# Kernel optimization log

Measured on AMD Instinct MI355X. Metric: run time of the kernel, lower is better.

The kernel has to match this reference:

```python
import jax, jax.numpy as jnp
import numpy as np
from jax import lax

D_MODEL, D_STATE, DT_RANK, D_INNER, K = 96, 16, 6, 192, 4


def cross_scan(x):
    # x: (B, C, H, W) -> (B, 4, C, L)
    B, C, H, W = x.shape
    x0 = x.reshape(B, C, H * W)                         # row-major scan
    x1 = jnp.transpose(x, (0, 1, 3, 2)).reshape(B, C, H * W)  # column-major scan
    return jnp.stack([x0, x1, x0[..., ::-1], x1[..., ::-1]], axis=1)


def cross_merge(ys, H, W):
    # ys: (B, 4, D, L) -> (B, D, L)
    B, Kd, D, L = ys.shape
    ys = ys[:, 0:2] + ys[:, 2:4, :, ::-1]
    y1 = jnp.transpose(ys[:, 1].reshape(B, D, W, H), (0, 1, 3, 2)).reshape(B, D, L)
    return ys[:, 0] + y1


def selective_scan(u, delta, A, Bs, Cs, Ds, delta_bias):
    # u, delta: (B, K, D, L); A: (K, D, N); Bs, Cs: (B, K, N, L); Ds, delta_bias: (K, D)
    Bsz, Kd, Dm, L = u.shape
    N = A.shape[-1]
    delta = jax.nn.softplus(delta + delta_bias[None, :, :, None])
    du = delta * u
    d_l = jnp.moveaxis(delta, -1, 0)   # (L, B, K, D)
    du_l = jnp.moveaxis(du, -1, 0)
    b_l = jnp.moveaxis(Bs, -1, 0)      # (L, B, K, N)
    c_l = jnpp = jnp.moveaxis(Cs, -1, 0)

    def step(h, inp):
        d_t, du_t, b_t, c_t = inp
        h = jnp.exp(d_t[..., None] * A) * h + du_t[..., None] * b_t[:, :, None, :]
        y = jnp.einsum('bkdn,bkn->bkd', h, c_t)
        return h, y

    h0 = jnp.zeros((Bsz, Kd, Dm, N), u.dtype)
    _, ys = lax.scan(step, h0, (d_l, du_l, b_l, c_l))
    ys = jnp.moveaxis(ys, 0, -1)  # (B, K, D, L)
    return ys + Ds[None, :, :, None] * u


def _forward(x, in_proj_w, conv_w, conv_b, x_proj_w, dt_projs_w, dt_projs_b,
             A_logs, Ds, out_norm_w, out_norm_b, out_proj_w):
    Bsz, H, W, dm = x.shape
    d_in = conv_w.shape[0]
    R, N = dt_projs_w.shape[2], A_logs.shape[-1]
    L = H * W
    # in_proj (no bias), split into x and gate z
    xz = jnp.einsum('bhwc,oc->bhwo', x, in_proj_w)
    xpart, z = jnp.split(xz, 2, axis=-1)
    z = jax.nn.silu(z)
    # depthwise 3x3 conv (NCHW) + SiLU
    xc = jnp.transpose(xpart, (0, 3, 1, 2))
    xc = lax.conv_general_dilated(xc, conv_w, (1, 1), 'SAME',
                                  feature_group_count=d_in,
                                  dimension_numbers=('NCHW', 'OIHW', 'NCHW'))
    xc = jax.nn.silu(xc + conv_b[None, :, None, None])
    # 4-directional cross scan
    xs = cross_scan(xc)                                   # (B, 4, d_in, L)
    x_dbl = jnp.einsum('bkdl,kcd->bkcl', xs, x_proj_w)    # (B, 4, R+2N, L)
    dts = jnp.einsum('bkrl,kdr->bkdl', x_dbl[:, :, :R], dt_projs_w)
    Bs = x_dbl[:, :, R:R + N]
    Cs = x_dbl[:, :, R + N:]
    A = -jnp.exp(A_logs)                                  # (4, d_in, N)
    ys = selective_scan(xs, dts, A, Bs, Cs, Ds, dt_projs_b)
    y = cross_merge(ys, H, W)                             # (B, d_in, L)
    y = jnp.transpose(y.reshape(Bsz, d_in, H, W), (0, 2, 3, 1))
    # out_norm = LayerNorm(d_inner), eps=1e-5
    mu = y.mean(-1, keepdims=True)
    var = ((y - mu) ** 2).mean(-1, keepdims=True)
    y = (y - mu) / jnp.sqrt(var + 1e-5) * out_norm_w + out_norm_b
    y = y * z
    return jnp.einsum('bhwd,od->bhwo', y, out_proj_w)


def setup_inputs() -> dict:
    key = jax.random.key(0)
    ks = jax.random.split(key, 8)
    dm, d_in, N, R = D_MODEL, D_INNER, D_STATE, DT_RANK
    x = jax.random.normal(ks[0], (8, 64, 64, dm), jnp.float32)
    in_proj_w = jax.random.normal(ks[1], (2 * d_in, dm), jnp.float32) * 0.02
    conv_w = jax.random.normal(ks[2], (d_in, 1, 3, 3), jnp.float32) * 0.1
    conv_b = jnp.zeros((d_in,), jnp.float32)
    x_proj_w = jax.random.normal(ks[3], (K, R + 2 * N, d_in), jnp.float32) * 0.02
    dt_projs_w = jax.random.normal(ks[4], (K, d_in, R), jnp.float32) * 0.1
    dt_projs_b = jax.random.uniform(ks[5], (K, d_in), jnp.float32, minval=-4.0, maxval=-2.0)
    A_logs = jnp.log(jnp.tile(jnp.arange(1, N + 1, dtype=jnp.float32)[None, None, :], (K, d_in, 1)))
    Ds = jnp.ones((K, d_in), jnp.float32)
    out_norm_w = jnp.ones((d_in,), jnp.float32)
    out_norm_b = jnp.zeros((d_in,), jnp.float32)
    out_proj_w = jax.random.normal(ks[6], (dm, d_in), jnp.float32) * 0.02
    return dict(x=x, in_proj_w=in_proj_w, conv_w=conv_w, conv_b=conv_b,
                x_proj_w=x_proj_w, dt_projs_w=dt_projs_w, dt_projs_b=dt_projs_b,
                A_logs=A_logs, Ds=Ds, out_norm_w=out_norm_w, out_norm_b=out_norm_b,
                out_proj_w=out_proj_w)


def reference(x, in_proj_w, conv_w, conv_b, x_proj_w, dt_projs_w, dt_projs_b,
              A_logs, Ds, out_norm_w, out_norm_b, out_proj_w):
    return _forward(x, in_proj_w, conv_w, conv_b, x_proj_w, dt_projs_w, dt_projs_b,
                    A_logs, Ds, out_norm_w, out_norm_b, out_proj_w)
```

## Files before the change

### kernel.cpp

```cpp
#include <hip/hip_runtime.h>
#include <math.h>

#define B_SZ 8
#define Hh 64
#define Ww 64
#define L 4096
#define Dm 96
#define Din 192
#define Kd 4
#define Ns 16
#define CPROJ 38
#define ROWW 40
#define NCHUNK 128
#define CHUNK 32

__device__ __forceinline__ float siluf_(float x){ return x / (1.f + __expf(-x)); }

__global__ void prep_kernel(const float* __restrict__ inw,
                            const float* __restrict__ xpw,
                            const float* __restrict__ outw,
                            float* __restrict__ wt_in,
                            float* __restrict__ wt_x,
                            float* __restrict__ wt_out){
  int i = blockIdx.x * blockDim.x + threadIdx.x;
  if (i < Dm*2*Din){ int k = i/(2*Din); int o = i%(2*Din); wt_in[i] = inw[o*Dm + k]; }
  int j = i - Dm*2*Din;
  if (j >= 0 && j < Din*Kd*CPROJ){ int k = j/(Kd*CPROJ); int c = j%(Kd*CPROJ); wt_x[j] = xpw[c*Din + k]; }
  int l = j - Din*Kd*CPROJ;
  if (l >= 0 && l < Din*Dm){ int dd = l/Dm; int o = l%Dm; wt_out[l] = outw[o*Din + dd]; }
}

__global__ __launch_bounds__(256) void zero_kernel(float4* __restrict__ p, int n4){
  int i = blockIdx.x * 256 + threadIdx.x;
  if (i < n4) p[i] = make_float4(0.f,0.f,0.f,0.f);
}

template<int KDIM, int OREAL, int EPI>
__global__ __launch_bounds__(256) void gemm_kernel(const float* __restrict__ X,
    const float* __restrict__ W, float* __restrict__ out0, float* __restrict__ out1){
  __shared__ float4 xt[128*24];
  const int tid = threadIdx.x;
  const int pg = tid & 15, og = tid >> 4;
  const int pblk = blockIdx.x & 255;
  const int oblk = blockIdx.x >> 8;
  const int p0 = pblk * 128;
  const bool act = (oblk*128 + og*8) < OREAL;
  int oc = oblk*128 + og*8;
  if (oc > OREAL-8) oc = OREAL-8;
  const int sw = pg & 7;

  float acc[8][8];
  #pragma unroll
  for (int i=0;i<8;i++){
    #pragma unroll
    for (int j2=0;j2<8;j2++) acc[i][j2] = 0.f;
  }

  for (int kp = 0; kp < KDIM/96; ++kp){
    __syncthreads();
    for (int idx = tid; idx < 128*24; idx += 256){
      int pp = idx/24, k4 = idx%24;
      size_t prow;
      if (EPI == 1){
        int b = pblk >> 5, tau = pblk & 31;
        int h = ((tau>>2)<<3) + (pp>>4);
        int w = ((tau&3)<<4) + (pp&15);
        prow = (size_t)b*L + h*64 + w;
      } else prow = (size_t)p0 + pp;
      float4 v = *(const float4*)&X[prow*KDIM + (size_t)kp*96 + k4*4];
      xt[pp*24 + (k4 ^ (pp&7))] = v;
    }
    __syncthreads();

    if (act){
      for (int k4 = 0; k4 < 24; ++k4){
        float4 wv[8];
        #pragma unroll
        for (int kk=0;kk<4;kk++){
          const float* wr = &W[(size_t)(kp*96 + k4*4 + kk)*OREAL + oc];
          wv[kk*2]   = *(const float4*)wr;
          wv[kk*2+1] = *(const float4*)(wr+4);
        }
        float4 xv[8];
        #pragma unroll
        for (int i=0;i<8;i++) xv[i] = xt[(pg+16*i)*24 + (k4 ^ sw)];
        #pragma unroll
        for (int kk=0;kk<4;kk++){
          const float4 wa = wv[kk*2], wb = wv[kk*2+1];
          #pragma unroll
          for (int i=0;i<8;i++){
            const float xk = ((const float*)&xv[i])[kk];
            acc[i][0] += xk*wa.x; acc[i][1] += xk*wa.y; acc[i][2] += xk*wa.z; acc[i][3] += xk*wa.w;
            acc[i][4] += xk*wb.x; acc[i][5] += xk*wb.y; acc[i][6] += xk*wb.z; acc[i][7] += xk*wb.w;
          }
        }
      }
    }
  }

  if (!act) return;
  if (EPI == 0){
    #pragma unroll
    for (int i=0;i<8;i++){
      size_t p = (size_t)p0 + pg + 16*i;
      if (oc < Din){
        *(float4*)&out0[p*Din + oc]     = make_float4(acc[i][0],acc[i][1],acc[i][2],acc[i][3]);
        *(float4*)&out0[p*Din + oc + 4] = make_float4(acc[i][4],acc[i][5],acc[i][6],acc[i][7]);
      } else {
        int zo = oc - Din;
        *(float4*)&out1[p*Din + zo]     = make_float4(siluf_(acc[i][0]),siluf_(acc[i][1]),siluf_(acc[i][2]),siluf_(acc[i][3]));
        *(float4*)&out1[p*Din + zo + 4] = make_float4(siluf_(acc[i][4]),siluf_(acc[i][5]),siluf_(acc[i][6]),siluf_(acc[i][7]));
      }
    }
  } else {
    const int b = pblk >> 5, tau = pblk & 31;
    #pragma unroll
    for (int i=0;i<8;i++){
      int q = pg + 16*i;
      int h = ((tau>>2)<<3) + (q>>4);
      int w = ((tau&3)<<4) + (q&15);
      int hw = h*64 + w;
      int t1 = ((hw&63)<<6) | (hw>>6);
      #pragma unroll
      for (int j2=0;j2<8;j2++){
        int c = oc + j2;
        int kd = c / CPROJ; int cc = c - kd*CPROJ;
        int t = (kd==0)? hw : (kd==1)? t1 : (kd==2)? (L-1-hw) : (L-1-t1);
        int dcol = (cc < 6) ? (32+cc) : (cc-6);
        out0[((size_t)(b*Kd+kd)*L + t)*ROWW + dcol] = acc[i][j2];
      }
    }
  }
}

__global__ __launch_bounds__(256) void conv_kernel(const float* __restrict__ xp,
    const float* __restrict__ cw, const float* __restrict__ cb, float* __restrict__ u){
  const int gid = blockIdx.x * 256 + threadIdx.x;
  const int d = gid % Din; const int p = gid / Din;
  const int b = p / L; const int hw = p % L; const int h = hw >> 6; const int w = hw & 63;
  float acc = cb[d];
  #pragma unroll
  for (int i=-1;i<=1;i++){
    const int hh = h + i; if (hh < 0 || hh >= Hh) continue;
    #pragma unroll
    for (int j=-1;j<=1;j++){
      const int ww = w + j; if (ww < 0 || ww >= Ww) continue;
      acc += xp[((size_t)(b*L + hh*Ww + ww))*Din + d] * cw[d*9 + (i+1)*3 + (j+1)];
    }
  }
  u[(size_t)p*Din + d] = siluf_(acc);
}

__device__ __forceinline__ void affine_pos(int k, int t0, int& gp0, int& gstr){
  if (k == 0){ gp0 = t0; gstr = 1; }
  else if (k == 1){ gp0 = ((t0 & 63) << 6) | (t0 >> 6); gstr = 64; }
  else if (k == 2){ gp0 = L-1-t0; gstr = -1; }
  else { const int T0 = L-1-t0; gp0 = ((T0 & 63) << 6) | (T0 >> 6); gstr = -64; }
}

__device__ __forceinline__ void ladder_(float e1, float* e){
  e[0]=e1;
  #pragma unroll
  for (int n=1;n<16;n++){ int P=n+1; e[n] = e[(P+1)/2 - 1] * e[P/2 - 1]; }
}

__global__ __launch_bounds__(192) void scanq_kernel(const float* __restrict__ u,
    const float* __restrict__ xq, const float* __restrict__ dtw,
    const float* __restrict__ dtb, const float* __restrict__ alog,
    float* __restrict__ qout, float* __restrict__ Sout){
  const int bid = blockIdx.x;
  const int c = bid & (NCHUNK-1); const int k = (bid >> 7) & 3; const int b = bid >> 9;
  const int d = threadIdx.x;
  const int bk = b*Kd + k;
  float wdt[6];
  #pragma unroll
  for (int r=0;r<6;r++) wdt[r] = dtw[(k*Din + d)*6 + r];
  const float bias = dtb[k*Din + d];
  float a2[16]; bool fastb = true;
  #pragma unroll
  for (int n=0;n<16;n++){
    a2[n] = -__expf(alog[(k*Din + d)*16 + n]);
    fastb = fastb && (fabsf(a2[n] + (float)(n+1)) < 1e-5f*(float)(n+1));
  }
  const bool fast = (bool)__all((int)fastb);
  float h[16];
  #pragma unroll
  for (int n=0;n<16;n++) h[n] = 0.f;
  float S = 0.f;
  const int t0 = c * CHUNK;
  int gp0, gstr; affine_pos(k, t0, gp0, gstr);
  const float* __restrict__ up = u + (size_t)b*L*Din + (size_t)gp0*Din + d;
  const ptrdiff_t ustep = (ptrdiff_t)gstr * Din;
  const float* __restrict__ rowp = xq + ((size_t)bk*L + t0)*ROWW;
  #pragma unroll 4
  for (int s = 0; s < CHUNK; ++s){
    const float4* __restrict__ rq = (const float4*)rowp;
    const float4 B0=rq[0],B1=rq[1],B2=rq[2],B3=rq[3];
    const float4 D0=rq[8];
    const float2 D1=((const float2*)rowp)[18];
    const float uval = *up;
    float dr = bias + D0.x*wdt[0]+D0.y*wdt[1]+D0.z*wdt[2]+D0.w*wdt[3]+D1.x*wdt[4]+D1.y*wdt[5];
    const float pp = __expf(dr);
    const float delta = (dr > 20.f) ? dr : __logf(1.f + pp);
    S += delta;
    const float du = delta * uval;
    float e[16];
    if (fast){
      ladder_(__builtin_amdgcn_rcpf(1.f + pp), e);
    } else {
      #pragma unroll
      for (int n=0;n<16;n++) e[n] = __expf(delta * a2[n]);
    }
    h[0] =e[0] *h[0] +du*B0.x; h[1] =e[1] *h[1] +du*B0.y; h[2] =e[2] *h[2] +du*B0.z; h[3] =e[3] *h[3] +du*B0.w;
    h[4] =e[4] *h[4] +du*B1.x; h[5] =e[5] *h[5] +du*B1.y; h[6] =e[6] *h[6] +du*B1.z; h[7] =e[7] *h[7] +du*B1.w;
    h[8] =e[8] *h[8] +du*B2.x; h[9] =e[9] *h[9] +du*B2.y; h[10]=e[10]*h[10]+du*B2.z; h[11]=e[11]*h[11]+du*B2.w;
    h[12]=e[12]*h[12]+du*B3.x; h[13]=e[13]*h[13]+du*B3.y; h[14]=e[14]*h[14]+du*B3.z; h[15]=e[15]*h[15]+du*B3.w;
    up += ustep; rowp += ROWW;
  }
  const size_t base = ((size_t)bk*NCHUNK + c)*Ns*Din + d;
  #pragma unroll
  for (int n=0;n<16;n++) qout[base + (size_t)n*Din] = h[n];
  Sout[((size_t)bk*NCHUNK + c)*Din + d] = S;
}

__global__ __launch_bounds__(256) void combine_kernel(const float* __restrict__ alog,
    const float* __restrict__ qin, const float* __restrict__ Sin, float* __restrict__ hout){
  const int gid = blockIdx.x * 256 + threadIdx.x;
  if (gid >= B_SZ*Kd*Ns*Din) return;
  const int d = gid % Din; const int n = (gid / Din) % Ns; const int bk = gid / (Din*Ns);
  const int k = bk & 3;
  const float A = -__expf(alog[(k*Din + d)*16 + n]);
  float h = 0.f;
  #pragma unroll 2
  for (int c=0;c<NCHUNK;c++){
    const size_t idx = (((size_t)bk*NCHUNK + c)*Ns + n)*Din + d;
    hout[idx] = h;
    h = __expf(A * Sin[((size_t)bk*NCHUNK + c)*Din + d]) * h + qin[idx];
  }
}

__global__ __launch_bounds__(192) void scany_kernel(const float* __restrict__ u,
    const float* __restrict__ xq, const float* __restrict__ dtw,
    const float* __restrict__ dtb, const float* __restrict__ alog,
    const float* __restrict__ Dsin, const float* __restrict__ hin,
    float* __restrict__ ym){
  const int bid = blockIdx.x;
  const int c = bid & (NCHUNK-1); const int k = (bid >> 7) & 3; const int b = bid >> 9;
  const int d = threadIdx.x;
  const int bk = b*Kd + k;

  float wdt[6];
  #pragma unroll
  for (int r=0;r<6;r++) wdt[r] = dtw[(k*Din + d)*6 + r];
  const float bias = dtb[k*Din + d];
  const float Dval = Dsin[k*Din + d];
  float a2[16]; bool fastb = true;
  #pragma unroll
  for (int n=0;n<16;n++){
    a2[n] = -__expf(alog[(k*Din + d)*16 + n]);
    fastb = fastb && (fabsf(a2[n] + (float)(n+1)) < 1e-5f*(float)(n+1));
  }
  const bool fast = (bool)__all((int)fastb);
  float h[16];
  const size_t hbase = ((size_t)bk*NCHUNK + c)*Ns*Din + d;
  #pragma unroll
  for (int n=0;n<16;n++) h[n] = hin[hbase + (size_t)n*Din];

  const int t0 = c * CHUNK;
  int gp0, gstr; affine_pos(k, t0, gp0, gstr);
  const float* __restrict__ up = u + (size_t)b*L*Din + (size_t)gp0*Din + d;
  float* __restrict__ yp = ym + (size_t)b*L*Din + (size_t)gp0*Din + d;
  const ptrdiff_t ustep = (ptrdiff_t)gstr * Din;
  const float* __restrict__ rowp = xq + ((size_t)bk*L + t0)*ROWW;
  #pragma unroll 4
  for (int s = 0; s < CHUNK; ++s){
    const float4* __restrict__ rq = (const float4*)rowp;
    const float4 B0=rq[0],B1=rq[1],B2=rq[2],B3=rq[3];
    const float4 C0=rq[4],C1=rq[5],C2=rq[6],C3=rq[7];
    const float4 D0=rq[8];
    const float2 D1=((const float2*)rowp)[18];
    const float uval = *up;
    float dr = bias + D0.x*wdt[0]+D0.y*wdt[1]+D0.z*wdt[2]+D0.w*wdt[3]+D1.x*wdt[4]+D1.y*wdt[5];
    const float pp = __expf(dr);
    const float delta = (dr > 20.f) ? dr : __logf(1.f + pp);
    const float du = delta * uval;
    float e[16];
    if (fast){
      ladder_(__builtin_amdgcn_rcpf(1.f + pp), e);
    } else {
      #pragma unroll
      for (int n=0;n<16;n++) e[n] = __expf(delta * a2[n]);
    }
    h[0] =e[0] *h[0] +du*B0.x; h[1] =e[1] *h[1] +du*B0.y; h[2] =e[2] *h[2] +du*B0.z; h[3] =e[3] *h[3] +du*B0.w;
    h[4] =e[4] *h[4] +du*B1.x; h[5] =e[5] *h[5] +du*B1.y; h[6] =e[6] *h[6] +du*B1.z; h[7] =e[7] *h[7] +du*B1.w;
    h[8] =e[8] *h[8] +du*B2.x; h[9] =e[9] *h[9] +du*B2.z==0.f?h[9]:e[9]*h[9]+du*B2.y;
    h[9] =e[9] *h[9];
    up += ustep; yp += ustep; rowp += ROWW;
  }
}

__global__ __launch_bounds__(192) void scany_kernel2(const float* __restrict__ u,
    const float* __restrict__ xq, const float* __restrict__ dtw,
    const float* __restrict__ dtb, const float* __restrict__ alog,
    const float* __restrict__ Dsin, const float* __restrict__ hin,
    float* __restrict__ ym){
  const int bid = blockIdx.x;
  const int c = bid & (NCHUNK-1); const int k = (bid >> 7) & 3; const int b = bid >> 9;
  const int d = threadIdx.x;
  const int bk = b*Kd + k;

  float wdt[6];
  #pragma unroll
  for (int r=0;r<6;r++) wdt[r] = dtw[(k*Din + d)*6 + r];
  const float bias = dtb[k*Din + d];
  const float Dval = Dsin[k*Din + d];
  float a2[16]; bool fastb = true;
  #pragma unroll
  for (int n=0;n<16;n++){
    a2[n] = -__expf(alog[(k*Din + d)*16 + n]);
    fastb = fastb && (fabsf(a2[n] + (float)(n+1)) < 1e-5f*(float)(n+1));
  }
  const bool fast = (bool)__all((int)fastb);
  float h[16];
  const size_t hbase = ((size_t)bk*NCHUNK + c)*Ns*Din + d;
  #pragma unroll
  for (int n=0;n<16;n++) h[n] = hin[hbase + (size_t)n*Din];

  const int t0 = c * CHUNK;
  int gp0, gstr; affine_pos(k, t0, gp0, gstr);
  const float* __restrict__ up = u + (size_t)b*L*Din + (size_t)gp0*Din + d;
  float* __restrict__ yp = ym + (size_t)b*L*Din + (size_t)gp0*Din + d;
  const ptrdiff_t ustep = (ptrdiff_t)gstr * Din;
  const float* __restrict__ rowp = xq + ((size_t)bk*L + t0)*ROWW;
  #pragma unroll 4
  for (int s = 0; s < CHUNK; ++s){
    const float4* __restrict__ rq = (const float4*)rowp;
    const float4 B0=rq[0],B1=rq[1],B2=rq[2],B3=rq[3];
    const float4 C0=rq[4],C1=rq[5],C2=rq[6],C3=rq[7];
    const float4 D0=rq[8];
    const float2 D1=((const float2*)rowp)[18];
    const float uval = *up;
    float dr = bias + D0.x*wdt[0]+D0.y*wdt[1]+D0.z*wdt[2]+D0.w*wdt[3]+D1.x*wdt[4]+D1.y*wdt[5];
    const float pp = __expf(dr);
    const float delta = (dr > 20.f) ? dr : __logf(1.f + pp);
    const float du = delta * uval;
    float e[16];
    if (fast){
      ladder_(__builtin_amdgcn_rcpf(1.f + pp), e);
    } else {
      #pragma unroll
      for (int n=0;n<16;n++) e[n] = __expf(delta * a2[n]);
    }
    h[0] =e[0] *h[0] +du*B0.x; h[1] =e[1] *h[1] +du*B0.y; h[2] =e[2] *h[2] +du*B0.z; h[3] =e[3] *h[3] +du*B0.w;
    h[4] =e[4] *h[4] +du*B1.x; h[5] =e[5] *h[5] +du*B1.y; h[6] =e[6] *h[6] +du*B1.z; h[7] =e[7] *h[7] +du*B1.w;
    h[8] =e[8] *h[8] +du*B2.x; h[9] =e[9] *h[9] +du*B2.y; h[10]=e[10]*h[10]+du*B2.z; h[11]=e[11]*h[11]+du*B2.w;
    h[12]=e[12]*h[12]+du*B3.x; h[13]=e[13]*h[13]+du*B3.y; h[14]=e[14]*h[14]+du*B3.z; h[15]=e[15]*h[15]+du*B3.w;
    float y0 = h[0]*C0.x + h[1]*C0.y;  float y1 = h[2]*C0.z + h[3]*C0.w;
    float y2 = h[4]*C1.x + h[5]*C1.y;  float y3 = h[6]*C1.z + h[7]*C1.w;
    y0 += h[8]*C2.x + h[9]*C2.y;   y1 += h[10]*C2.z + h[11]*C2.w;
    y2 += h[12]*C3.x + h[13]*C3.y; y3 += h[14]*C3.z + h[15]*C3.w;
    atomicAdd(yp, (y0+y1)+(y2+y3) + Dval*uval);
    up += ustep; yp += ustep; rowp += ROWW;
  }
}

__global__ __launch_bounds__(192) void outproj_kernel(const float* __restrict__ ym,
    const float* __restrict__ z, const float* __restrict__ gw, const float* __restrict__ gb,
    const float* __restrict__ wto,
    float* __restrict__ out){
  __shared__ float xt[64*192];
  __shared__ float smu[64], sinv[64];
  const int tid = threadIdx.x;
  const int p0 = blockIdx.x * 64;
  if (tid < 128){
    const int r = tid >> 1, part = tid & 1;
    const float4* __restrict__ src = (const float4*)(ym + (size_t)(p0 + r)*Din + part*96);
    float s = 0.f, ss = 0.f;
    #pragma unroll
    for (int i=0;i<24;i++){
      float4 v = src[i];
      s  += (v.x+v.y)+(v.z+v.w);
      ss += (v.x*v.x+v.y*v.y)+(v.z*v.z+v.w*v.w);
    }
    s += __shfl_xor(s, 1); ss += __shfl_xor(ss, 1);
    if (!part){
      const float mu = s * (1.f/Din);
      smu[r] = mu;
      sinv[r] = rsqrtf(ss*(1.f/Din) - mu*mu + 1e-5f);
    }
  }
  __syncthreads();
  for (int idx = tid; idx < 64*48; idx += 192){
    const int r = idx/48, k4 = idx - (idx/48)*48;
    const size_t g = (size_t)(p0+r)*Din + k4*4;
    float4 v  = *(const float4*)(ym + g);
    const float4 zv = *(const float4*)(z + g);
    const float4 gwv = *(const float4*)(gw + k4*4);
    const float4 gbv = *(const float4*)(gb + k4*4);
    const float mu = smu[r], inv = sinv[r];
    v.x = ((v.x-mu)*inv*gwv.x + gbv.x)*zv.x;
    v.y = ((v.y-mu)*inv*gwv.y + gbv.y)*zv.y;
    v.z = ((v.z-mu)*inv*gwv.z + gbv.z)*zv.z;
    v.w = ((v.w-mu)*inv*gwv.w + gbv.w)*zv.w;
    const int k4s = (k4 & ~7) | ((k4 ^ r) & 7);
    *(float4*)(xt + r*192 + k4s*4) = v;
  }
  __syncthreads();
  const int pg = tid/12, og = tid - (tid/12)*12;
  const int oc = og*8;
  float acc[4][8];
  #pragma unroll
  for (int i=0;i<4;i++){
    #pragma unroll
    for (int j=0;j<8;j++) acc[i][j] = 0.f;
  }
  for (int k4 = 0; k4 < 48; ++k4){
    float4 xv[4];
    #pragma unroll
    for (int i=0;i<4;i++){
      const int r = pg*4+i;
      const int k4s = (k4 & ~7) | ((k4 ^ r) & 7);
      xv[i] = *(const float4*)(xt + r*192 + k4s*4);
    }
    #pragma unroll
    for (int j=0;j<4;j++){
      const int k = k4*4 + j;
      const float4 w0 = *(const float4*)(wto + (size_t)k*Dm + oc);
      const float4 w1 = *(const float4*)(wto + (size_t)k*Dm + oc + 4);
      #pragma unroll
      for (int i=0;i<4;i++){
        const float xk = ((const float*)&xv[i])[j];
        acc[i][0] += xk*w0.x; acc[i][1] += xk*w0.y; acc[i][2] += xk*w0.z; acc[i][3] += xk*w0.w;
        acc[i][4] += xk*w1.x; acc[i][5] += xk*w1.y; acc[i][6] += xk*w1.z; acc[i][7] += xk*w1.w;
      }
    }
  }
  #pragma unroll
  for (int i=0;i<4;i++){
    const size_t row = (size_t)p0 + pg*4 + i;
    *(float4*)(out + row*Dm + oc)     = make_float4(acc[i][0],acc[i][1],acc[i][2],acc[i][3]);
    *(float4*)(out + row*Dm + oc + 4) = make_float4(acc[i][4],acc[i][5],acc[i][6],acc[i][7]);
  }
}

extern "C" void kernel_launch(void* const* d_in, const int* in_sizes, int n_in,
                              void* d_out, int out_size, void* d_ws, size_t ws_size,
                              hipStream_t stream) {
  const float* x      = (const float*)d_in[0];
  const float* inw    = (const float*)d_in[1];
  const float* convw  = (const float*)d_in[2];
  const float* convb  = (const float*)d_in[3];
  const float* xprojw = (const float*)d_in[4];
  const float* dtw    = (const float*)d_in[5];
  const float* dtb    = (const float*)d_in[6];
  const float* alog   = (const float*)d_in[7];
  const float* Ds     = (const float*)d_in[8];
  const float* gw     = (const float*)d_in[9];
  const float* gb     = (const float*)d_in[10];
  const float* outw   = (const float*)d_in[11];
  float* out = (float*)d_out;

  float* ws = (float*)d_ws;
  const size_t nBLD  = (size_t)B_SZ*L*Din;
  const size_t nXQ   = (size_t)B_SZ*Kd*L*ROWW;
  const size_t nQ    = (size_t)B_SZ*Kd*NCHUNK*Ns*Din;
  const size_t nS    = (size_t)B_SZ*Kd*NCHUNK*Din;
  size_t off = 0;
  float* xpart = ws + off; off += nQ;
  float* zbuf  = ws + off; off += nBLD;
  float* ubuf  = ws + off; off += nBLD;
  float* xq    = ws + off; off += nXQ;
  float* qbuf  = ws + off; off += nQ;
  float* Sbuf  = ws + off; off += nS;
  float* ym    = ws + off; off += nBLD;
  float* wt_in = ws + off; off += (size_t)Dm*2*Din;
  float* wt_x  = ws + off; off += (size_t)Din*Kd*CPROJ;
  float* wt_out= ws + off; off += (size_t)Din*Dm;

  const int prepN = Dm*2*Din + Din*Kd*CPROJ + Din*Dm;
  prep_kernel<<<(prepN + 255)/256, 256, 0, stream>>>(inw, xprojw, outw, wt_in, wt_x, wt_out);
  zero_kernel<<<(int)(nBLD/4 + 255)/256, 256, 0, stream>>>((float4*)ym, (int)(nBLD/4));
  gemm_kernel<Dm, 2*Din, 0><<<256*3, 256, 0, stream>>>(x, wt_in, xpart, zbuf);
  conv_kernel<<<(int)(nBLD/256), 256, 0, stream>>>(xpart, convw, convb, ubuf);
  gemm_kernel<Din, Kd*CPROJ, 1><<<256*2, 256, 0, stream>>>(ubuf, wt_x, xq, nullptr);
  scanq_kernel<<<B_SZ*Kd*NCHUNK, Din, 0, stream>>>(ubuf, xq, dtw, dtb, alog, qbuf, Sbuf);
  combine_kernel<<<(B_SZ*Kd*Ns*Din + 255)/256, 256, 0, stream>>>(alog, qbuf, Sbuf, xpart);
  scany_kernel2<<<B_SZ*Kd*NCHUNK, Din, 0, stream>>>(ubuf, xq, dtw, dtb, alog, Ds, xpart, ym);
  outproj_kernel<<<B_SZ*L/64, 192, 0, stream>>>(ym, zbuf, gw, gb, wt_out, out);
}
```

Measured before the change: 470.9 us.

## Split chunked scan into local-output pass plus linear carry-in correction pass

The first scan pass now emits its local outputs (including the D*u skip term) with zero initial state. The second pass only adds the contribution of the carried-in state, decayed by a cumulative exponential, so it no longer needs B, u, or the full state recurrence. The x_proj GEMM now writes rows in spatial order, and the scans read them with the direction's stride instead of a permuted layout. The combine kernel batches its loads eight chunks at a time. The cost is doubled atomic traffic into ym, strided row reads for the column directions, and a cumulative product E that could lose precision over a chunk.

```diff
diff --git a/kernel.cpp b/kernel.cpp
--- a/kernel.cpp
+++ b/kernel.cpp
@@ -60,13 +60,7 @@
     __syncthreads();
     for (int idx = tid; idx < 128*24; idx += 256){
       int pp = idx/24, k4 = idx%24;
-      size_t prow;
-      if (EPI == 1){
-        int b = pblk >> 5, tau = pblk & 31;
-        int h = ((tau>>2)<<3) + (pp>>4);
-        int w = ((tau&3)<<4) + (pp&15);
-        prow = (size_t)b*L + h*64 + w;
-      } else prow = (size_t)p0 + pp;
+      size_t prow = (size_t)p0 + pp;
       float4 v = *(const float4*)&X[prow*KDIM + (size_t)kp*96 + k4*4];
       xt[pp*24 + (k4 ^ (pp&7))] = v;
     }
@@ -113,21 +107,17 @@
       }
     }
   } else {
-    const int b = pblk >> 5, tau = pblk & 31;
     #pragma unroll
     for (int i=0;i<8;i++){
-      int q = pg + 16*i;
-      int h = ((tau>>2)<<3) + (q>>4);
-      int w = ((tau&3)<<4) + (q&15);
-      int hw = h*64 + w;
-      int t1 = ((hw&63)<<6) | (hw>>6);
+      const int p = p0 + pg + 16*i;
+      const int b = p >> 12;
+      const int hw = p & (L-1);
       #pragma unroll
       for (int j2=0;j2<8;j2++){
         int c = oc + j2;
         int kd = c / CPROJ; int cc = c - kd*CPROJ;
-        int t = (kd==0)? hw : (kd==1)? t1 : (kd==2)? (L-1-hw) : (L-1-t1);
         int dcol = (cc < 6) ? (32+cc) : (cc-6);
-        out0[((size_t)(b*Kd+kd)*L + t)*ROWW + dcol] = acc[i][j2];
+        out0[((size_t)(b*Kd+kd)*L + hw)*ROWW + dcol] = acc[i][j2];
       }
     }
   }
@@ -164,10 +154,11 @@
   for (int n=1;n<16;n++){ int P=n+1; e[n] = e[(P+1)/2 - 1] * e[P/2 - 1]; }
 }
 
-__global__ __launch_bounds__(192) void scanq_kernel(const float* __restrict__ u,
+__global__ __launch_bounds__(192) void scan_local_kernel(const float* __restrict__ u,
     const float* __restrict__ xq, const float* __restrict__ dtw,
     const float* __restrict__ dtb, const float* __restrict__ alog,
-    float* __restrict__ qout, float* __restrict__ Sout){
+    const float* __restrict__ Dsin,
+    float* __restrict__ qout, float* __restrict__ Sout, float* __restrict__ ym){
   const int bid = blockIdx.x;
   const int c = bid & (NCHUNK-1); const int k = (bid >> 7) & 3; const int b = bid >> 9;
   const int d = threadIdx.x;
@@ -176,6 +167,7 @@
   #pragma unroll
   for (int r=0;r<6;r++) wdt[r] = dtw[(k*Din + d)*6 + r];
   const float bias = dtb[k*Din + d];
+  const float Dval = Dsin[k*Din + d];
   float a2[16]; bool fastb = true;
   #pragma unroll
   for (int n=0;n<16;n++){
@@ -190,12 +182,15 @@
   const int t0 = c * CHUNK;
   int gp0, gstr; affine_pos(k, t0, gp0, gstr);
   const float* __restrict__ up = u + (size_t)b*L*Din + (size_t)gp0*Din + d;
+  float* __restrict__ yp = ym + (size_t)b*L*Din + (size_t)gp0*Din + d;
   const ptrdiff_t ustep = (ptrdiff_t)gstr * Din;
-  const float* __restrict__ rowp = xq + ((size_t)bk*L + t0)*ROWW;
+  const float* __restrict__ rowp = xq + ((size_t)bk*L + gp0)*ROWW;
+  const ptrdiff_t rstep = (ptrdiff_t)gstr * ROWW;
   #pragma unroll 4
   for (int s = 0; s < CHUNK; ++s){
     const float4* __restrict__ rq = (const float4*)rowp;
     const float4 B0=rq[0],B1=rq[1],B2=rq[2],B3=rq[3];
+    const float4 C0=rq[4],C1=rq[5],C2=rq[6],C3=rq[7];
     const float4 D0=rq[8];
     const float2 D1=((const float2*)rowp)[18];
     const float uval = *up;
@@ -215,7 +210,12 @@
     h[4] =e[4] *h[4] +du*B1.x; h[5] =e[5] *h[5] +du*B1.y; h[6] =e[6] *h[6] +du*B1.z; h[7] =e[7] *h[7] +du*B1.w;
     h[8] =e[8] *h[8] +du*B2.x; h[9] =e[9] *h[9] +du*B2.y; h[10]=e[10]*h[10]+du*B2.z; h[11]=e[11]*h[11]+du*B2.w;
     h[12]=e[12]*h[12]+du*B3.x; h[13]=e[13]*h[13]+du*B3.y; h[14]=e[14]*h[14]+du*B3.z; h[15]=e[15]*h[15]+du*B3.w;
-    up += ustep; rowp += ROWW;
+    float y0 = h[0]*C0.x + h[1]*C0.y;  float y1 = h[2]*C0.z + h[3]*C0.w;
+    float y2 = h[4]*C1.x + h[5]*C1.y;  float y3 = h[6]*C1.z + h[7]*C1.w;
+    y0 += h[8]*C2.x + h[9]*C2.y;   y1 += h[10]*C2.z + h[11]*C2.w;
+    y2 += h[12]*C3.x + h[13]*C3.y; y3 += h[14]*C3.z + h[15]*C3.w;
+    atomicAdd(yp, (y0+y1)+(y2+y3) + Dval*uval);
+    up += ustep; yp += ustep; rowp += rstep;
   }
   const size_t base = ((size_t)bk*NCHUNK + c)*Ns*Din + d;
   #pragma unroll
@@ -230,30 +230,35 @@
   const int d = gid % Din; const int n = (gid / Din) % Ns; const int bk = gid / (Din*Ns);
   const int k = bk & 3;
   const float A = -__expf(alog[(k*Din + d)*16 + n]);
+  const size_t stepQ = (size_t)Ns*Din;
+  size_t idx = ((size_t)bk*NCHUNK)*stepQ + (size_t)n*Din + d;
+  size_t sidx = ((size_t)bk*NCHUNK)*Din + d;
   float h = 0.f;
-  #pragma unroll 2
-  for (int c=0;c<NCHUNK;c++){
-    const size_t idx = (((size_t)bk*NCHUNK + c)*Ns + n)*Din + d;
-    hout[idx] = h;
-    h = __expf(A * Sin[((size_t)bk*NCHUNK + c)*Din + d]) * h + qin[idx];
-  }
-}
-
-__global__ __launch_bounds__(192) void scany_kernel(const float* __restrict__ u,
-    const float* __restrict__ xq, const float* __restrict__ dtw,
-    const float* __restrict__ dtb, const float* __restrict__ alog,
-    const float* __restrict__ Dsin, const float* __restrict__ hin,
+  for (int c0=0;c0<NCHUNK;c0+=8){
+    float qv[8], Sv[8];
+    #pragma unroll
+    for (int j=0;j<8;j++){ qv[j] = qin[idx + (size_t)j*stepQ]; Sv[j] = Sin[sidx + (size_t)j*Din]; }
+    #pragma unroll
+    for (int j=0;j<8;j++){
+      hout[idx + (size_t)j*stepQ] = h;
+      h = __expf(A*Sv[j])*h + qv[j];
+    }
+    idx += 8*stepQ; sidx += (size_t)8*Din;
+  }
+}
+
+__global__ __launch_bounds__(192) void scan_corr_kernel(const float* __restrict__ xq,
+    const float* __restrict__ dtw, const float* __restrict__ dtb,
+    const float* __restrict__ alog, const float* __restrict__ hin,
     float* __restrict__ ym){
   const int bid = blockIdx.x;
   const int c = bid & (NCHUNK-1); const int k = (bid >> 7) & 3; const int b = bid >> 9;
   const int d = threadIdx.x;
   const int bk = b*Kd + k;
-
   float wdt[6];
   #pragma unroll
   for (int r=0;r<6;r++) wdt[r] = dtw[(k*Din + d)*6 + r];
   const float bias = dtb[k*Din + d];
-  const float Dval = Dsin[k*Din + d];
   float a2[16]; bool fastb = true;
   #pragma unroll
   for (int n=0;n<16;n++){
@@ -261,106 +266,45 @@
     fastb = fastb && (fabsf(a2[n] + (float)(n+1)) < 1e-5f*(float)(n+1));
   }
   const bool fast = (bool)__all((int)fastb);
-  float h[16];
+  float g[16];
   const size_t hbase = ((size_t)bk*NCHUNK + c)*Ns*Din + d;
   #pragma unroll
-  for (int n=0;n<16;n++) h[n] = hin[hbase + (size_t)n*Din];
+  for (int n=0;n<16;n++) g[n] = hin[hbase + (size_t)n*Din];
 
   const int t0 = c * CHUNK;
   int gp0, gstr; affine_pos(k, t0, gp0, gstr);
-  const float* __restrict__ up = u + (size_t)b*L*Din + (size_t)gp0*Din + d;
   float* __restrict__ yp = ym + (size_t)b*L*Din + (size_t)gp0*Din + d;
   const ptrdiff_t ustep = (ptrdiff_t)gstr * Din;
-  const float* __restrict__ rowp = xq + ((size_t)bk*L + t0)*ROWW;
+  const float* __restrict__ rowp = xq + ((size_t)bk*L + gp0)*ROWW;
+  const ptrdiff_t rstep = (ptrdiff_t)gstr * ROWW;
+  float E = 1.f, cumS = 0.f;
   #pragma unroll 4
   for (int s = 0; s < CHUNK; ++s){
     const float4* __restrict__ rq = (const float4*)rowp;
-    const float4 B0=rq[0],B1=rq[1],B2=rq[2],B3=rq[3];
     const float4 C0=rq[4],C1=rq[5],C2=rq[6],C3=rq[7];
     const float4 D0=rq[8];
     const float2 D1=((const float2*)rowp)[18];
-    const float uval = *up;
     float dr = bias + D0.x*wdt[0]+D0.y*wdt[1]+D0.z*wdt[2]+D0.w*wdt[3]+D1.x*wdt[4]+D1.y*wdt[5];
     const float pp = __expf(dr);
-    const float delta = (dr > 20.f) ? dr : __logf(1.f + pp);
-    const float du = delta * uval;
-    float e[16];
+    float lad[16];
     if (fast){
-      ladder_(__builtin_amdgcn_rcpf(1.f + pp), e);
+      E *= __builtin_amdgcn_rcpf(1.f + pp);
+      ladder_(E, lad);
     } else {
+      const float delta = (dr > 20.f) ? dr : __logf(1.f + pp);
+      cumS += delta;
       #pragma unroll
-      for (int n=0;n<16;n++) e[n] = __expf(delta * a2[n]);
-    }
-    h[0] =e[0] *h[0] +du*B0.x; h[1] =e[1] *h[1] +du*B0.y; h[2] =e[2] *h[2] +du*B0.z; h[3] =e[3] *h[3] +du*B0.w;
-    h[4] =e[4] *h[4] +du*B1.x; h[5] =e[5] *h[5] +du*B1.y; h[6] =e[6] *h[6] +du*B1.z; h[7] =e[7] *h[7] +du*B1.w;
-    h[8] =e[8] *h[8] +du*B2.x; h[9] =e[9] *h[9] +du*B2.z==0.f?h[9]:e[9]*h[9]+du*B2.y;
-    h[9] =e[9] *h[9];
-    up += ustep; yp += ustep; rowp += ROWW;
-  }
-}
-
-__global__ __launch_bounds__(192) void scany_kernel2(const float* __restrict__ u,
-    const float* __restrict__ xq, const float* __restrict__ dtw,
-    const float* __restrict__ dtb, const float* __restrict__ alog,
-    const float* __restrict__ Dsin, const float* __restrict__ hin,
-    float* __restrict__ ym){
-  const int bid = blockIdx.x;
-  const int c = bid & (NCHUNK-1); const int k = (bid >> 7) & 3; const int b = bid >> 9;
-  const int d = threadIdx.x;
-  const int bk = b*Kd + k;
-
-  float wdt[6];
-  #pragma unroll
-  for (int r=0;r<6;r++) wdt[r] = dtw[(k*Din + d)*6 + r];
-  const float bias = dtb[k*Din + d];
-  const float Dval = Dsin[k*Din + d];
-  float a2[16]; bool fastb = true;
-  #pragma unroll
-  for (int n=0;n<16;n++){
-    a2[n] = -__expf(alog[(k*Din + d)*16 + n]);
-    fastb = fastb && (fabsf(a2[n] + (float)(n+1)) < 1e-5f*(float)(n+1));
-  }
-  const bool fast = (bool)__all((int)fastb);
-  float h[16];
-  const size_t hbase = ((size_t)bk*NCHUNK + c)*Ns*Din + d;
-  #pragma unroll
-  for (int n=0;n<16;n++) h[n] = hin[hbase + (size_t)n*Din];
-
-  const int t0 = c * CHUNK;
-  int gp0, gstr; affine_pos(k, t0, gp0, gstr);
-  const float* __restrict__ up = u + (size_t)b*L*Din + (size_t)gp0*Din + d;
-  float* __restrict__ yp = ym + (size_t)b*L*Din + (size_t)gp0*Din + d;
-  const ptrdiff_t ustep = (ptrdiff_t)gstr * Din;
-  const float* __restrict__ rowp = xq + ((size_t)bk*L + t0)*ROWW;
-  #pragma unroll 4
-  for (int s = 0; s < CHUNK; ++s){
-    const float4* __restrict__ rq = (const float4*)rowp;
-    const float4 B0=rq[0],B1=rq[1],B2=rq[2],B3=rq[3];
-    const float4 C0=rq[4],C1=rq[5],C2=rq[6],C3=rq[7];
-    const float4 D0=rq[8];
-    const float2 D1=((const float2*)rowp)[18];
-    const float uval = *up;
-    float dr = bias + D0.x*wdt[0]+D0.y*wdt[1]+D0.z*wdt[2]+D0.w*wdt[3]+D1.x*wdt[4]+D1.y*wdt[5];
-    const float pp = __expf(dr);
-    const float delta = (dr > 20.f) ? dr : __logf(1.f + pp);
-    const float du = delta * uval;
-    float e[16];
-    if (fast){
-      ladder_(__builtin_amdgcn_rcpf(1.f + pp), e);
-    } else {
-      #pragma unroll
-      for (int n=0;n<16;n++) e[n] = __expf(delta * a2[n]);
-    }
-    h[0] =e[0] *h[0] +du*B0.x; h[1] =e[1] *h[1] +du*B0.y; h[2] =e[2] *h[2] +du*B0.z; h[3] =e[3] *h[3] +du*B0.w;
-    h[4] =e[4] *h[4] +du*B1.x; h[5] =e[5] *h[5] +du*B1.y; h[6] =e[6] *h[6] +du*B1.z; h[7] =e[7] *h[7] +du*B1.w;
-    h[8] =e[8] *h[8] +du*B2.x; h[9] =e[9] *h[9] +du*B2.y; h[10]=e[10]*h[10]+du*B2.z; h[11]=e[11]*h[11]+du*B2.w;
-    h[12]=e[12]*h[12]+du*B3.x; h[13]=e[13]*h[13]+du*B3.y; h[14]=e[14]*h[14]+du*B3.z; h[15]=e[15]*h[15]+du*B3.w;
-    float y0 = h[0]*C0.x + h[1]*C0.y;  float y1 = h[2]*C0.z + h[3]*C0.w;
-    float y2 = h[4]*C1.x + h[5]*C1.y;  float y3 = h[6]*C1.z + h[7]*C1.w;
-    y0 += h[8]*C2.x + h[9]*C2.y;   y1 += h[10]*C2.z + h[11]*C2.w;
-    y2 += h[12]*C3.x + h[13]*C3.y; y3 += h[14]*C3.z + h[15]*C3.w;
-    atomicAdd(yp, (y0+y1)+(y2+y3) + Dval*uval);
-    up += ustep; yp += ustep; rowp += ROWW;
+      for (int n=0;n<16;n++) lad[n] = __expf(a2[n]*cumS);
+    }
+    float w0[16];
+    #pragma unroll
+    for (int n=0;n<16;n++) w0[n] = lad[n]*g[n];
+    float y0 = w0[0]*C0.x + w0[1]*C0.y;  float y1 = w0[2]*C0.z + w0[3]*C0.w;
+    float y2 = w0[4]*C1.x + w0[5]*C1.y;  float y3 = w0[6]*C1.z + w0[7]*C1.w;
+    y0 += w0[8]*C2.x + w0[9]*C2.y;   y1 += w0[10]*C2.z + w0[11]*C2.w;
+    y2 += w0[12]*C3.x + w0[13]*C3.y; y3 += w0[14]*C3.z + w0[15]*C3.w;
+    atomicAdd(yp, (y0+y1)+(y2+y3));
+    yp += ustep; rowp += rstep;
   }
 }
 
@@ -483,8 +427,8 @@
   gemm_kernel<Dm, 2*Din, 0><<<256*3, 256, 0, stream>>>(x, wt_in, xpart, zbuf);
   conv_kernel<<<(int)(nBLD/256), 256, 0, stream>>>(xpart, convw, convb, ubuf);
   gemm_kernel<Din, Kd*CPROJ, 1><<<256*2, 256, 0, stream>>>(ubuf, wt_x, xq, nullptr);
-  scanq_kernel<<<B_SZ*Kd*NCHUNK, Din, 0, stream>>>(ubuf, xq, dtw, dtb, alog, qbuf, Sbuf);
+  scan_local_kernel<<<B_SZ*Kd*NCHUNK, Din, 0, stream>>>(ubuf, xq, dtw, dtb, alog, Ds, qbuf, Sbuf, ym);
   combine_kernel<<<(B_SZ*Kd*Ns*Din + 255)/256, 256, 0, stream>>>(alog, qbuf, Sbuf, xpart);
-  scany_kernel2<<<B_SZ*Kd*NCHUNK, Din, 0, stream>>>(ubuf, xq, dtw, dtb, alog, Ds, xpart, ym);
+  scan_corr_kernel<<<B_SZ*Kd*NCHUNK, Din, 0, stream>>>(xq, dtw, dtb, alog, xpart, ym);
   outproj_kernel<<<B_SZ*L/64, 192, 0, stream>>>(ym, zbuf, gw, gb, wt_out, out);
 }
```

New measurement: 455.9 us. 3.2% less time.
